# Kernel optimization log

Hardware: AMD Instinct MI355X
Metric: run time of the kernel (lower is better)

Reference implementation:

```python
import jax, jax.numpy as jnp
import numpy as np

VOCAB = 50000
D = 256          # vector_dim == hidden size
SEQ = 128
BATCH = 4096
NUM_CLASSES = 5


def setup_inputs() -> dict:
    key = jax.random.key(0)
    ks = jax.random.split(key, 8)
    x = jax.random.randint(ks[0], (BATCH, SEQ), 0, VOCAB, dtype=jnp.int64)
    scale = 1.0 / np.sqrt(D)
    emb = jax.random.normal(ks[1], (VOCAB, D), dtype=jnp.float32)
    emb = emb.at[0].set(0.0)  # padding_idx=0 row is zero
    W_ih = jax.random.uniform(ks[2], (D, D), jnp.float32, -scale, scale)
    W_hh = jax.random.uniform(ks[3], (D, D), jnp.float32, -scale, scale)
    b_ih = jax.random.uniform(ks[4], (D,), jnp.float32, -scale, scale)
    b_hh = jax.random.uniform(ks[5], (D,), jnp.float32, -scale, scale)
    W_cls = jax.random.uniform(ks[6], (NUM_CLASSES, D), jnp.float32, -scale, scale)
    b_cls = jax.random.uniform(ks[7], (NUM_CLASSES,), jnp.float32, -scale, scale)
    return {"x": x, "emb": emb, "W_ih": W_ih, "W_hh": W_hh,
            "b_ih": b_ih, "b_hh": b_hh, "W_cls": W_cls, "b_cls": b_cls}


def reference(x, emb, W_ih, W_hh, b_ih, b_hh, W_cls, b_cls):
    # Embedding lookup: [B, S, D]
    xe = emb[x]
    # Precompute input projections for all timesteps in one GEMM.
    x_proj = jnp.einsum("bsd,hd->bsh", xe, W_ih) + b_ih + b_hh  # [B, S, D]

    def step(h, xp_t):
        h = jnp.tanh(xp_t + h @ W_hh.T)
        return h, None

    h0 = jnp.zeros((x.shape[0], W_hh.shape[0]), dtype=xe.dtype)
    # scan over time axis: [S, B, D]
    h_last, _ = jax.lax.scan(step, h0, jnp.swapaxes(x_proj, 0, 1))
    # classifier on last step
    return h_last @ W_cls.T + b_cls  # [B, 5]
```

## Files before the change

### kernel.cpp

```cpp
#include <hip/hip_runtime.h>


typedef __attribute__((ext_vector_type(8))) short bf16x8;
typedef __attribute__((ext_vector_type(4))) float f32x4;

#define VOCAB 50000
#define NBLK_EMB 512
#define LDS_STRIDE 264

__device__ __align__(256) unsigned short g_P[VOCAB * 256];

static __device__ __forceinline__ float bf2f(unsigned short u) {
    union { unsigned int i; float f; } v; v.i = ((unsigned int)u) << 16; return v.f;
}
static __device__ __forceinline__ float bfbits2f(unsigned int zext_u16) {
    union { unsigned int i; float f; } v; v.i = zext_u16 << 16; return v.f;
}
static __device__ __forceinline__ unsigned short f2bf_rne(float f) {
    union { float f; unsigned int i; } v; v.f = f;
    unsigned int r = v.i + 0x7FFFu + ((v.i >> 16) & 1u);
    return (unsigned short)(r >> 16);
}
static __device__ __forceinline__ unsigned short f2bf_fast(float f) {
    union { float f; unsigned int i; } v; v.f = f;
    return (unsigned short)((v.i + 0x8000u) >> 16);
}
static __device__ __forceinline__ bf16x8 cvt8(float4 a, float4 b) {
    bf16x8 r;
    r[0] = (short)f2bf_rne(a.x); r[1] = (short)f2bf_rne(a.y);
    r[2] = (short)f2bf_rne(a.z); r[3] = (short)f2bf_rne(a.w);
    r[4] = (short)f2bf_rne(b.x); r[5] = (short)f2bf_rne(b.y);
    r[6] = (short)f2bf_rne(b.z); r[7] = (short)f2bf_rne(b.w);
    return r;
}
static __device__ __forceinline__ bf16x8 load8_bf(const float* __restrict__ p) {
    return cvt8(((const float4*)p)[0], ((const float4*)p)[1]);
}
static __device__ __forceinline__ float fast_tanh(float x) {
    x = __builtin_amdgcn_fmed3f(x, -8.f, 8.f);
    float e = __expf(2.f * x);
    return __builtin_fmaf(-2.f, __builtin_amdgcn_rcpf(e + 1.f), 1.f);
}
static __device__ __forceinline__ void barrier_lds_only() {
    asm volatile("s_waitcnt lgkmcnt(0)\n\ts_barrier" ::: "memory");
}

__global__ __launch_bounds__(256)
void emb_proj_kernel(const float* __restrict__ emb,
                     const float* __restrict__ W_ih,
                     const float* __restrict__ b_ih,
                     const float* __restrict__ b_hh)
{
    __shared__ __align__(16) unsigned short tin[2][16 * LDS_STRIDE];
    const int tid  = threadIdx.x;
    const int lane = tid & 63;
    const int wid  = tid >> 6;
    const int n0   = wid * 64;
    const int row  = tid >> 4, seg = tid & 15;
    const int l15  = lane & 15;
    const int quad = lane >> 4;

    bf16x8 wf[4][8];
    float  bias[4];
    #pragma unroll
    for (int nt = 0; nt < 4; ++nt) {
        int n = n0 + nt * 16 + l15;
        bias[nt] = b_ih[n] + b_hh[n];
        #pragma unroll
        for (int kt = 0; kt < 8; ++kt)
            wf[nt][kt] = load8_bf(W_ih + n * 256 + quad * 8 + kt * 32);
    }

    const int b = blockIdx.x;
    float4 pf[2][4];

    {
        const float4* s0 = (const float4*)(emb + ((size_t)b * 16 + row) * 256 + seg * 16);
        pf[0][0] = s0[0]; pf[0][1] = s0[1]; pf[0][2] = s0[2]; pf[0][3] = s0[3];
        int t1 = b + NBLK_EMB;
        if (t1 < 3125) {
            const float4* s1 = (const float4*)(emb + ((size_t)t1 * 16 + row) * 256 + seg * 16);
            pf[1][0] = s1[0]; pf[1][1] = s1[1]; pf[1][2] = s1[2]; pf[1][3] = s1[3];
        }
    }

    #pragma unroll
    for (int i = 0; i < 7; ++i) {
        int tile = b + i * NBLK_EMB;
        if (tile < 3125) {
            *(bf16x8*)(&tin[i & 1][row * LDS_STRIDE + seg * 16])     = cvt8(pf[i & 1][0], pf[i & 1][1]);
            *(bf16x8*)(&tin[i & 1][row * LDS_STRIDE + seg * 16 + 8]) = cvt8(pf[i & 1][2], pf[i & 1][3]);
            int tf = tile + 2 * NBLK_EMB;
            if (tf < 3125) {
                const float4* s = (const float4*)(emb + ((size_t)tf * 16 + row) * 256 + seg * 16);
                pf[i & 1][0] = s[0]; pf[i & 1][1] = s[1]; pf[i & 1][2] = s[2]; pf[i & 1][3] = s[3];
            }
            barrier_lds_only();

            f32x4 acc[4];
            #pragma unroll
            for (int nt = 0; nt < 4; ++nt) acc[nt] = (f32x4){0.f, 0.f, 0.f, 0.f};
            #pragma unroll
            for (int kt = 0; kt < 8; ++kt) {
                bf16x8 a = *(bf16x8*)(&tin[i & 1][l15 * LDS_STRIDE + quad * 8 + kt * 32]);
                #pragma unroll
                for (int nt = 0; nt < 4; ++nt)
                    acc[nt] = __builtin_amdgcn_mfma_f32_16x16x32_bf16(a, wf[nt][kt], acc[nt], 0, 0, 0);
            }
            unsigned short* prow = g_P + ((size_t)tile * 16 + quad * 4) * 256 + n0;
            #pragma unroll
            for (int nt = 0; nt < 4; ++nt) {
                #pragma unroll
                for (int r = 0; r < 4; ++r)
                    prow[r * 256 + nt * 16 + l15] = f2bf_rne(acc[nt][r] + bias[nt]);
            }
        }
    }
}

__global__ __launch_bounds__(512, 2)
void rnn_kernel(const int* __restrict__ x,
                const float* __restrict__ W_hh,
                const float* __restrict__ W_cls,
                const float* __restrict__ b_cls,
                float* __restrict__ out)
{
    __shared__ __align__(16) unsigned short h_lds[2][16 * 256];
    __shared__ __align__(16) int tok_t[128 * 16];
    __shared__ __align__(16) float wcls_lds[5 * 256];
    __shared__ float bcls_lds[5];

    const int tid  = threadIdx.x;
    const int lane = tid & 63;
    const int wid  = tid >> 6;
    const int b0   = blockIdx.x * 16;
    const int n0   = wid * 32;
    const int l15  = lane & 15;
    const int quad = lane >> 4;

    bf16x8 wf[2][8];
    #pragma unroll
    for (int nt = 0; nt < 2; ++nt) {
        int n = n0 + nt * 16 + l15;
        #pragma unroll
        for (int kt = 0; kt < 8; ++kt)
            wf[nt][kt] = load8_bf(W_hh + n * 256 + quad * 8 + kt * 32);
    }

    {
        int row = tid & 15, tq = tid >> 4;
        int4 v = *(const int4*)(x + (size_t)(b0 + row) * 128 + tq * 4);
        tok_t[(tq * 4 + 0) * 16 + row] = v.x;
        tok_t[(tq * 4 + 1) * 16 + row] = v.y;
        tok_t[(tq * 4 + 2) * 16 + row] = v.z;
        tok_t[(tq * 4 + 3) * 16 + row] = v.w;
    }
    if (tid < 320) ((float4*)wcls_lds)[tid] = ((const float4*)W_cls)[tid];
    if (tid < 5)   bcls_lds[tid] = b_cls[tid];
    #pragma unroll
    for (int i = 0; i < 4; ++i) ((unsigned int*)h_lds[0])[tid + i * 512] = 0;

    int aoff[8];
    #pragma unroll
    for (int kt = 0; kt < 8; ++kt)
        aoff[kt] = l15 * 512 + (((quad + 4 * kt) ^ l15) << 4);
    int woff[8];
    #pragma unroll
    for (int nt = 0; nt < 2; ++nt)
        #pragma unroll
        for (int r = 0; r < 4; ++r) {
            int row = quad * 4 + r;
            int g   = (n0 >> 3) + nt * 2 + (l15 >> 3);
            woff[nt * 4 + r] = row * 512 + ((g ^ row) << 4) + (l15 & 7) * 2;
        }

    const unsigned int colByte = (unsigned int)(n0 + l15) * 2;

    unsigned int gA[8], gB[8];
    #pragma unroll
    for (int r = 0; r < 4; ++r) {
        const int* xr = x + (size_t)(b0 + quad * 4 + r) * 128;
        const unsigned short* p0 = g_P + (size_t)xr[0] * 256 + n0 + l15;
        const unsigned short* p1 = g_P + (size_t)xr[1] * 256 + n0 + l15;
        gA[r] = p0[0]; gA[4 + r] = p0[16];
        gB[r] = p1[0]; gB[4 + r] = p1[16];
    }
    __syncthreads();

    char* const h0 = (char*)&h_lds[0][0];

    auto step = [&](const char* hA, char* hW, unsigned int* g, int t) {
        f32x4 acc0 = { bfbits2f(g[0]), bfbits2f(g[1]), bfbits2f(g[2]), bfbits2f(g[3]) };
        f32x4 acc1 = { bfbits2f(g[4]), bfbits2f(g[5]), bfbits2f(g[6]), bfbits2f(g[7]) };
        if (t + 2 < 128) {
            int4 tk = *(const int4*)&tok_t[(t + 2) * 16 + quad * 4];
            const unsigned short* r0 = (const unsigned short*)((const char*)g_P + ((unsigned int)tk.x * 512 + colByte));
            const unsigned short* r1 = (const unsigned short*)((const char*)g_P + ((unsigned int)tk.y * 512 + colByte));
            const unsigned short* r2 = (const unsigned short*)((const char*)g_P + ((unsigned int)tk.z * 512 + colByte));
            const unsigned short* r3 = (const unsigned short*)((const char*)g_P + ((unsigned int)tk.w * 512 + colByte));
            g[0] = r0[0]; g[4] = r0[16];
            g[1] = r1[0]; g[5] = r1[16];
            g[2] = r2[0]; g[6] = r2[16];
            g[3] = r3[0]; g[7] = r3[16];
        }
        #pragma unroll
        for (int kt = 0; kt < 8; ++kt) {
            bf16x8 a = *(const bf16x8*)(hA + aoff[kt]);
            acc0 = __builtin_amdgcn_mfma_f32_16x16x32_bf16(a, wf[0][kt], acc0, 0, 0, 0);
            acc1 = __builtin_amdgcn_mfma_f32_16x16x32_bf16(a, wf[1][kt], acc1, 0, 0, 0);
        }
        #pragma unroll
        for (int r = 0; r < 4; ++r) {
            *(unsigned short*)(hW + woff[r])     = f2bf_fast(fast_tanh(acc0[r]));
            *(unsigned short*)(hW + woff[4 + r]) = f2bf_fast(fast_tanh(acc1[r]));
        }
    };

    #pragma unroll 1
    for (int t2 = 0; t2 < 64; ++t2) {
        step(h0,        h0 + 8192, gA, 2 * t2);
        __syncthreads();
        step(h0 + 8192, h0,        gB, 2 * t2 + 1);
        __syncthreads();
    }

    if (tid < 320) {
        int q = tid & 3, p = tid >> 2;
        int row = p / 5, c = p - row * 5;
        float acc = 0.f;
        #pragma unroll
        for (int kk = 0; kk < 64; ++kk) {
            int k = q * 64 + kk;
            int off = row * 512 + ((((k >> 3) ^ row)) << 4) + (k & 7) * 2;
            acc += bf2f(*(const unsigned short*)(h0 + off)) * wcls_lds[c * 256 + k];
        }
        acc += __shfl_xor(acc, 1);
        acc += __shfl_xor(acc, 2);
        if (q == 0) out[(size_t)(b0 + row) * 5 + c] = acc + bcls_lds[c];
    }
}

extern "C" void kernel_launch(void* const* d_in, const int* in_sizes, int n_in,
                              void* d_out, int out_size, void* d_ws, size_t ws_size,
                              hipStream_t stream)
{
    const int*   x     = (const int*)d_in[0];
    const float* emb   = (const float*)d_in[1];
    const float* W_ih  = (const float*)d_in[2];
    const float* W_hh  = (const float*)d_in[3];
    const float* b_ih  = (const float*)d_in[4];
    const float* b_hh  = (const float*)d_in[5];
    const float* W_cls = (const float*)d_in[6];
    const float* b_cls = (const float*)d_in[7];
    float*       out   = (float*)d_out;
    (void)d_ws; (void)ws_size;

    emb_proj_kernel<<<NBLK_EMB, 256, 0, stream>>>(emb, W_ih, b_ih, b_hh);
    rnn_kernel<<<256, 512, 0, stream>>>(x, W_hh, W_cls, b_cls, out);
}
```

Baseline: 232.9 us.

## Stream embedding tiles to LDS with direct global-to-LDS loads and 4-stage buffering

The embedding projection kernel now loads fp32 embedding rows straight into a 4-deep LDS staging ring with global_load_lds, replacing the register prefetch, convert and ds_write path. Conversion to bf16 moves to the point where MFMA operands are read from LDS. Hand-tuned vmcnt waits keep up to two tiles in flight. In exchange LDS use roughly quadruples to fp32 staging, and correctness depends on the exact vmcnt counts matching the number of outstanding loads and stores.

```diff
diff --git a/kernel.cpp b/kernel.cpp
--- a/kernel.cpp
+++ b/kernel.cpp
@@ -6,7 +6,7 @@
 
 #define VOCAB 50000
 #define NBLK_EMB 512
-#define LDS_STRIDE 264
+#define NTILES 3125
 
 __device__ __align__(256) unsigned short g_P[VOCAB * 256];
 
@@ -51,12 +51,11 @@
                      const float* __restrict__ b_ih,
                      const float* __restrict__ b_hh)
 {
-    __shared__ __align__(16) unsigned short tin[2][16 * LDS_STRIDE];
+    __shared__ __align__(1024) float stage[4][16][260];
     const int tid  = threadIdx.x;
     const int lane = tid & 63;
     const int wid  = tid >> 6;
     const int n0   = wid * 64;
-    const int row  = tid >> 4, seg = tid & 15;
     const int l15  = lane & 15;
     const int quad = lane >> 4;
 
@@ -72,29 +71,32 @@
     }
 
     const int b = blockIdx.x;
-    float4 pf[2][4];
-
-    {
-        const float4* s0 = (const float4*)(emb + ((size_t)b * 16 + row) * 256 + seg * 16);
-        pf[0][0] = s0[0]; pf[0][1] = s0[1]; pf[0][2] = s0[2]; pf[0][3] = s0[3];
-        int t1 = b + NBLK_EMB;
-        if (t1 < 3125) {
-            const float4* s1 = (const float4*)(emb + ((size_t)t1 * 16 + row) * 256 + seg * 16);
-            pf[1][0] = s1[0]; pf[1][1] = s1[1]; pf[1][2] = s1[2]; pf[1][3] = s1[3];
-        }
-    }
+
+    auto issue = [&](int t, int j) {
+        if (t < NTILES) {
+            #pragma unroll
+            for (int rr = 0; rr < 4; ++rr) {
+                int row = wid * 4 + rr;
+                const float* g = emb + ((size_t)t * 16 + row) * 256 + lane * 4;
+                __builtin_amdgcn_global_load_lds(
+                    (const __attribute__((address_space(1))) void*)g,
+                    (__attribute__((address_space(3))) void*)&stage[j][row][0],
+                    16, 0, 0);
+            }
+        }
+    };
+
+    issue(b,            0);
+    issue(b + NBLK_EMB, 1);
 
     #pragma unroll
     for (int i = 0; i < 7; ++i) {
         int tile = b + i * NBLK_EMB;
-        if (tile < 3125) {
-            *(bf16x8*)(&tin[i & 1][row * LDS_STRIDE + seg * 16])     = cvt8(pf[i & 1][0], pf[i & 1][1]);
-            *(bf16x8*)(&tin[i & 1][row * LDS_STRIDE + seg * 16 + 8]) = cvt8(pf[i & 1][2], pf[i & 1][3]);
-            int tf = tile + 2 * NBLK_EMB;
-            if (tf < 3125) {
-                const float4* s = (const float4*)(emb + ((size_t)tf * 16 + row) * 256 + seg * 16);
-                pf[i & 1][0] = s[0]; pf[i & 1][1] = s[1]; pf[i & 1][2] = s[2]; pf[i & 1][3] = s[3];
-            }
+        if (tile < NTILES) {
+            issue(b + (i + 2) * NBLK_EMB, (i + 2) & 3);
+            if (i == 0)      asm volatile("s_waitcnt vmcnt(0)"  ::: "memory");
+            else if (i == 1) asm volatile("s_waitcnt vmcnt(16)" ::: "memory");
+            else             asm volatile("s_waitcnt vmcnt(32)" ::: "memory");
             barrier_lds_only();
 
             f32x4 acc[4];
@@ -102,7 +104,9 @@
             for (int nt = 0; nt < 4; ++nt) acc[nt] = (f32x4){0.f, 0.f, 0.f, 0.f};
             #pragma unroll
             for (int kt = 0; kt < 8; ++kt) {
-                bf16x8 a = *(bf16x8*)(&tin[i & 1][l15 * LDS_STRIDE + quad * 8 + kt * 32]);
+                float4 u = *(const float4*)&stage[i & 3][l15][quad * 8 + kt * 32];
+                float4 v = *(const float4*)&stage[i & 3][l15][quad * 8 + kt * 32 + 4];
+                bf16x8 a = cvt8(u, v);
                 #pragma unroll
                 for (int nt = 0; nt < 4; ++nt)
                     acc[nt] = __builtin_amdgcn_mfma_f32_16x16x32_bf16(a, wf[nt][kt], acc[nt], 0, 0, 0);
```

New measurement: 239.7 us. 1.03x slower.
